# Optimization experiments

Hardware: AMD Instinct MI355X
Metric: run time of the kernel (lower is better)

The kernel has to match this reference:

```python
import jax, jax.numpy as jnp
import numpy as np

EMA = 0.999
EPS = 1e-8


def setup_inputs() -> dict:
    key = jax.random.key(0)
    k1, k2, k3 = jax.random.split(key, 3)
    B, z_dim, H, W = 16, 64, 32, 32
    M = 4096
    N = B * H * W
    return {
        "z": jax.random.normal(k1, (B, z_dim, H, W), dtype=jnp.float32),
        "e": jax.random.normal(k2, (M, z_dim), dtype=jnp.float32),
        "belong": jax.random.uniform(k3, (N, M), dtype=jnp.float32),
        "log_sigma": jnp.zeros((1,), dtype=jnp.float32),
        "max_distance": jnp.ones((1, M), dtype=jnp.float32),
        "distance_p": 2,
    }


def reference(z, e, belong, log_sigma, max_distance, distance_p):
    B, z_dim, H, W = z.shape
    # [B, z_dim, H, W] -> [N, z_dim], N = B*H*W
    zf = jnp.transpose(z, (0, 2, 3, 1)).reshape(-1, z_dim)
    # pairwise L2 distance via GEMM expansion: ||z||^2 + ||e||^2 - 2 z.e
    d2 = (jnp.sum(zf * zf, axis=1, keepdims=True)
          + jnp.sum(e * e, axis=1)[None, :]
          - 2.0 * (zf @ e.T))                      # [N, M]
    distance = jnp.sqrt(jnp.maximum(d2, 0.0))
    # EMA update of per-code max distance (buffer, no grad in original)
    batch_max = jnp.max(belong * distance, axis=0, keepdims=True)  # [1, M]
    new_max = EMA * max_distance + (1.0 - EMA) * batch_max
    new_max = jax.lax.stop_gradient(jnp.clip(new_max, EPS, None))
    p = float(distance_p)
    distance = jnp.where(distance < new_max,
                         distance ** (2.0 / p),
                         distance ** (2.0 * p))
    alpha = -1.0 / (2.0 * jnp.exp(log_sigma) ** 2)  # shape (1,)
    lse = jax.scipy.special.logsumexp(alpha * distance, axis=0)  # [M]
    loss = -jnp.mean(lse) + z_dim * log_sigma  # shape (1,), as in torch
    return loss
```

## Files before the change

kernel.cpp:

```cpp
#include <hip/hip_runtime.h>
#include <hip/hip_bf16.h>

#define ZD   64
#define MM   4096
#define NN   16384
#define HWSZ 1024
#define BB   16

typedef __bf16 bf16x8 __attribute__((ext_vector_type(8)));
typedef float  f32x4  __attribute__((ext_vector_type(4)));

#define EMA_C 0.999f
#define EPS_C 1e-8f

__global__ __launch_bounds__(256) void k_prep_e(const float* __restrict__ e,
                                                __hip_bfloat16* __restrict__ ebf,
                                                float* __restrict__ en2,
                                                unsigned* __restrict__ bmax,
                                                unsigned* __restrict__ dmin,
                                                float* __restrict__ sume) {
    int tid = threadIdx.x;
    int gid = blockIdx.x * 256 + tid;
    if (gid < MM) {
        bmax[gid] = 0u;
        dmin[gid] = 0x7f800000u;
        sume[gid] = 0.f;
    }
    int wave = tid >> 6, lane = tid & 63;
    int row = blockIdx.x * 4 + wave;
    if (row < MM) {
        float v = e[row * ZD + lane];
        __hip_bfloat16 b = __float2bfloat16(v);
        ebf[row * ZD + lane] = b;
        float q = __bfloat162float(b);
        float s = q * q;
        for (int off = 32; off; off >>= 1) s += __shfl_xor(s, off);
        if (lane == 0) en2[row] = s;
    }
}

__global__ __launch_bounds__(256) void k_prep_z(const float* __restrict__ z,
                                                __hip_bfloat16* __restrict__ zf,
                                                float* __restrict__ zn2) {
    __shared__ float tile[64][65];
    __shared__ float part[4][64];
    int b   = blockIdx.x;
    int hw0 = blockIdx.y * 64;
    int tid = threadIdx.x;
    int tx = tid & 63, ty = tid >> 6;
    const float* zp = z + (size_t)b * (ZD * HWSZ);
#pragma unroll
    for (int kk = 0; kk < 16; kk++) {
        int k = kk * 4 + ty;
        tile[k][tx] = zp[(size_t)k * HWSZ + hw0 + tx];
    }
    __syncthreads();
#pragma unroll
    for (int i = 0; i < 16; i++) {
        int li = tid + i * 256;
        int ln = li >> 6, lk = li & 63;
        int n = b * HWSZ + hw0 + ln;
        zf[(size_t)n * ZD + lk] = __float2bfloat16(tile[lk][ln]);
    }
    float s = 0.f;
#pragma unroll
    for (int kk = 0; kk < 16; kk++) {
        float q = __bfloat162float(__float2bfloat16(tile[ty + kk * 4][tx]));
        s += q * q;
    }
    part[ty][tx] = s;
    __syncthreads();
    if (tid < 64) {
        float t = part[0][tid] + part[1][tid] + part[2][tid] + part[3][tid];
        zn2[b * HWSZ + hw0 + tid] = t;
    }
}

__global__ __launch_bounds__(256) void k_pass1(const __hip_bfloat16* __restrict__ zf,
                                               const __hip_bfloat16* __restrict__ ebf,
                                               const float* __restrict__ zn2,
                                               const float* __restrict__ en2,
                                               const float* __restrict__ belong,
                                               unsigned* __restrict__ bmax,
                                               unsigned* __restrict__ dmin) {
    int tid = threadIdx.x;
    int wave = tid >> 6, lane = tid & 63;
    int l16 = lane & 15, lq = lane >> 4;
    int wn = wave >> 1, wm = wave & 1;
    int n0 = blockIdx.x * 64 + wn * 32;
    int m0 = blockIdx.y * 128 + wm * 64;

    const bf16x8* zfv = reinterpret_cast<const bf16x8*>(zf);
    const bf16x8* ebv = reinterpret_cast<const bf16x8*>(ebf);

    bf16x8 Af[2][2], Bf[4][2];
#pragma unroll
    for (int i = 0; i < 2; i++)
#pragma unroll
        for (int h = 0; h < 2; h++)
            Af[i][h] = zfv[(size_t)(n0 + i * 16 + l16) * 8 + h * 4 + lq];
#pragma unroll
    for (int j = 0; j < 4; j++)
#pragma unroll
        for (int h = 0; h < 2; h++)
            Bf[j][h] = ebv[(size_t)(m0 + j * 16 + l16) * 8 + h * 4 + lq];

    f32x4 acc[2][4];
#pragma unroll
    for (int i = 0; i < 2; i++)
#pragma unroll
        for (int j = 0; j < 4; j++) {
            acc[i][j] = (f32x4){0.f, 0.f, 0.f, 0.f};
            acc[i][j] = __builtin_amdgcn_mfma_f32_16x16x32_bf16(Af[i][0], Bf[j][0], acc[i][j], 0, 0, 0);
            acc[i][j] = __builtin_amdgcn_mfma_f32_16x16x32_bf16(Af[i][1], Bf[j][1], acc[i][j], 0, 0, 0);
        }

    float zn2v[2][4];
#pragma unroll
    for (int i = 0; i < 2; i++)
#pragma unroll
        for (int r = 0; r < 4; r++)
            zn2v[i][r] = zn2[n0 + i * 16 + lq * 4 + r];

    __shared__ unsigned smax[128], smin[128];
    if (tid < 128) { smax[tid] = 0u; smin[tid] = 0x7f800000u; }
    __syncthreads();

#pragma unroll
    for (int j = 0; j < 4; j++) {
        float en2v = en2[m0 + j * 16 + l16];
        float vmax = 0.f, vmin = 3.4e38f;
#pragma unroll
        for (int i = 0; i < 2; i++)
#pragma unroll
            for (int r = 0; r < 4; r++) {
                float d2 = zn2v[i][r] + en2v - 2.f * acc[i][j][r];
                float d = sqrtf(fmaxf(d2, 0.f));
                int n = n0 + i * 16 + lq * 4 + r;
                float bel = belong[(size_t)n * MM + (m0 + j * 16 + l16)];
                vmax = fmaxf(vmax, bel * d);
                vmin = fminf(vmin, d);
            }
        vmax = fmaxf(vmax, __shfl_xor(vmax, 16));
        vmax = fmaxf(vmax, __shfl_xor(vmax, 32));
        vmin = fminf(vmin, __shfl_xor(vmin, 16));
        vmin = fminf(vmin, __shfl_xor(vmin, 32));
        if (lane < 16) {
            int ml = wm * 64 + j * 16 + lane;
            atomicMax(&smax[ml], __float_as_uint(vmax));
            atomicMin(&smin[ml], __float_as_uint(vmin));
        }
    }
    __syncthreads();
    if (tid < 128) {
        atomicMax(&bmax[blockIdx.y * 128 + tid], smax[tid]);
        atomicMin(&dmin[blockIdx.y * 128 + tid], smin[tid]);
    }
}

__global__ __launch_bounds__(256) void k_mid(const unsigned* __restrict__ bmax,
                                             const unsigned* __restrict__ dmin,
                                             const float* __restrict__ max_distance,
                                             const float* __restrict__ log_sigma,
                                             const int* __restrict__ pp,
                                             float* __restrict__ nmax,
                                             float* __restrict__ refs) {
    int m = blockIdx.x * 256 + threadIdx.x;
    if (m >= MM) return;
    float bm = __uint_as_float(bmax[m]);
    float dm = __uint_as_float(dmin[m]);
    float nm = fmaxf(EMA_C * max_distance[m] + (1.f - EMA_C) * bm, EPS_C);
    int p = pp[0];
    float tlow;
    if (p == 2) {
        float d4  = (dm * dm) * (dm * dm);
        float nm4 = (nm * nm) * (nm * nm);
        tlow = (dm < nm) ? fminf(dm, nm4) : d4;
    } else {
        float e1 = 2.f / (float)p, e2 = 2.f * (float)p;
        tlow = (dm < nm) ? fminf(powf(dm, e1), powf(nm, e2)) : powf(dm, e2);
    }
    float alpha = -0.5f * expf(-2.f * log_sigma[0]);
    nmax[m] = nm;
    refs[m] = alpha * tlow;
}

__global__ __launch_bounds__(256) void k_pass2(const __hip_bfloat16* __restrict__ zf,
                                               const __hip_bfloat16* __restrict__ ebf,
                                               const float* __restrict__ zn2,
                                               const float* __restrict__ en2,
                                               const float* __restrict__ nmax,
                                               const float* __restrict__ refs,
                                               const float* __restrict__ log_sigma,
                                               const int* __restrict__ pp,
                                               float* __restrict__ sume) {
    int tid = threadIdx.x;
    int wave = tid >> 6, lane = tid & 63;
    int l16 = lane & 15, lq = lane >> 4;
    int wn = wave >> 1, wm = wave & 1;
    int n0 = blockIdx.x * 64 + wn * 32;
    int m0 = blockIdx.y * 128 + wm * 64;

    const bf16x8* zfv = reinterpret_cast<const bf16x8*>(zf);
    const bf16x8* ebv = reinterpret_cast<const bf16x8*>(ebf);

    bf16x8 Af[2][2], Bf[4][2];
#pragma unroll
    for (int i = 0; i < 2; i++)
#pragma unroll
        for (int h = 0; h < 2; h++)
            Af[i][h] = zfv[(size_t)(n0 + i * 16 + l16) * 8 + h * 4 + lq];
#pragma unroll
    for (int j = 0; j < 4; j++)
#pragma unroll
        for (int h = 0; h < 2; h++)
            Bf[j][h] = ebv[(size_t)(m0 + j * 16 + l16) * 8 + h * 4 + lq];

    f32x4 acc[2][4];
#pragma unroll
    for (int i = 0; i < 2; i++)
#pragma unroll
        for (int j = 0; j < 4; j++) {
            acc[i][j] = (f32x4){0.f, 0.f, 0.f, 0.f};
            acc[i][j] = __builtin_amdgcn_mfma_f32_16x16x32_bf16(Af[i][0], Bf[j][0], acc[i][j], 0, 0, 0);
            acc[i][j] = __builtin_amdgcn_mfma_f32_16x16x32_bf16(Af[i][1], Bf[j][1], acc[i][j], 0, 0, 0);
        }

    float zn2v[2][4];
#pragma unroll
    for (int i = 0; i < 2; i++)
#pragma unroll
        for (int r = 0; r < 4; r++)
            zn2v[i][r] = zn2[n0 + i * 16 + lq * 4 + r];

    float alpha = -0.5f * expf(-2.f * log_sigma[0]);
    int p = pp[0];
    bool p2 = (p == 2);
    float e1 = 2.f / (float)p, e2 = 2.f * (float)p;

    __shared__ float ssum[128];
    if (tid < 128) ssum[tid] = 0.f;
    __syncthreads();

#pragma unroll
    for (int j = 0; j < 4; j++) {
        float en2v = en2[m0 + j * 16 + l16];
        float nmv = nmax[m0 + j * 16 + l16];
        float rfv = refs[m0 + j * 16 + l16];
        float csum = 0.f;
#pragma unroll
        for (int i = 0; i < 2; i++)
#pragma unroll
            for (int r = 0; r < 4; r++) {
                float d2c = fmaxf(zn2v[i][r] + en2v - 2.f * acc[i][j][r], 0.f);
                float d = sqrtf(d2c);
                float t;
                if (p2) t = (d < nmv) ? d : d2c * d2c;
                else    t = powf(d, (d < nmv) ? e1 : e2);
                csum += expf(alpha * t - rfv);
            }
        csum += __shfl_xor(csum, 16);
        csum += __shfl_xor(csum, 32);
        if (lane < 16) atomicAdd(&ssum[wm * 64 + j * 16 + lane], csum);
    }
    __syncthreads();
    if (tid < 128) atomicAdd(&sume[blockIdx.y * 128 + tid], ssum[tid]);
}

__global__ __launch_bounds__(256) void k_final(const float* __restrict__ refs,
                                               const float* __restrict__ sume,
                                               const float* __restrict__ log_sigma,
                                               float* __restrict__ out) {
    __shared__ float red[4];
    int tid = threadIdx.x;
    float a = 0.f;
    for (int m = tid; m < MM; m += 256)
        a += refs[m] + logf(fmaxf(sume[m], 1e-30f));
    for (int off = 32; off; off >>= 1) a += __shfl_xor(a, off);
    int wave = tid >> 6, lane = tid & 63;
    if (lane == 0) red[wave] = a;
    __syncthreads();
    if (tid == 0) {
        float t = red[0] + red[1] + red[2] + red[3];
        out[0] = -t / (float)MM + (float)ZD * log_sigma[0];
    }
}

extern "C" void kernel_launch(void* const* d_in, const int* in_sizes, int n_in,
                              void* d_out, int out_size, void* d_ws, size_t ws_size,
                              hipStream_t stream) {
    const float* z            = (const float*)d_in[0];
    const float* e            = (const float*)d_in[1];
    const float* belong       = (const float*)d_in[2];
    const float* log_sigma    = (const float*)d_in[3];
    const float* max_distance = (const float*)d_in[4];
    const int*   pp           = (const int*)d_in[5];
    float* out = (float*)d_out;

    char* ws = (char*)d_ws;
    __hip_bfloat16* zf  = (__hip_bfloat16*)(ws + 0);
    __hip_bfloat16* ebf = (__hip_bfloat16*)(ws + 2097152);
    float*    zn2  = (float*)(ws + 2621440);
    float*    en2  = (float*)(ws + 2686976);
    unsigned* bmax = (unsigned*)(ws + 2703360);
    unsigned* dmin = (unsigned*)(ws + 2719744);
    float*    nmax = (float*)(ws + 2736128);
    float*    refs = (float*)(ws + 2752512);
    float*    sume = (float*)(ws + 2768896);

    k_prep_e<<<1024, 256, 0, stream>>>(e, ebf, en2, bmax, dmin, sume);
    k_prep_z<<<dim3(BB, HWSZ / 64), 256, 0, stream>>>(z, zf, zn2);
    k_pass1<<<dim3(NN / 64, MM / 128), 256, 0, stream>>>(zf, ebf, zn2, en2, belong, bmax, dmin);
    k_mid<<<MM / 256, 256, 0, stream>>>(bmax, dmin, max_distance, log_sigma, pp, nmax, refs);
    k_pass2<<<dim3(NN / 64, MM / 128), 256, 0, stream>>>(zf, ebf, zn2, en2, nmax, refs, log_sigma, pp, sume);
    k_final<<<1, 256, 0, stream>>>(refs, sume, log_sigma, out);
}
```

Before: 503.4 us.

## Transpose pass1 tiling for vectorized belong loads and fuse prep/mid kernels

Pass1 swaps the MFMA operand roles so each lane reads four consecutive belong values as one nontemporal 16-byte load, with the max/min reductions reworked to match the new layout. The two prep kernels are merged into one launch. The mid kernel is folded into pass2, which recomputes the per-code EMA max and reference in shared memory. Pass2 compares squared distances to skip sqrt on one branch and uses fast exp. The aim is to cut launch overhead and make the dominant 256MB belong stream more efficient, at the cost of redundant per-block mid computation and fast-math exp precision.

```diff
diff --git a/kernel.cpp b/kernel.cpp
--- a/kernel.cpp
+++ b/kernel.cpp
@@ -13,66 +13,68 @@
 #define EMA_C 0.999f
 #define EPS_C 1e-8f
 
-__global__ __launch_bounds__(256) void k_prep_e(const float* __restrict__ e,
-                                                __hip_bfloat16* __restrict__ ebf,
-                                                float* __restrict__ en2,
-                                                unsigned* __restrict__ bmax,
-                                                unsigned* __restrict__ dmin,
-                                                float* __restrict__ sume) {
-    int tid = threadIdx.x;
-    int gid = blockIdx.x * 256 + tid;
-    if (gid < MM) {
-        bmax[gid] = 0u;
-        dmin[gid] = 0x7f800000u;
-        sume[gid] = 0.f;
-    }
-    int wave = tid >> 6, lane = tid & 63;
-    int row = blockIdx.x * 4 + wave;
-    if (row < MM) {
-        float v = e[row * ZD + lane];
-        __hip_bfloat16 b = __float2bfloat16(v);
-        ebf[row * ZD + lane] = b;
-        float q = __bfloat162float(b);
-        float s = q * q;
-        for (int off = 32; off; off >>= 1) s += __shfl_xor(s, off);
-        if (lane == 0) en2[row] = s;
-    }
-}
-
-__global__ __launch_bounds__(256) void k_prep_z(const float* __restrict__ z,
-                                                __hip_bfloat16* __restrict__ zf,
-                                                float* __restrict__ zn2) {
+__global__ __launch_bounds__(256) void k_prep(const float* __restrict__ z,
+                                              const float* __restrict__ e,
+                                              __hip_bfloat16* __restrict__ zf,
+                                              __hip_bfloat16* __restrict__ ebf,
+                                              float* __restrict__ zn2,
+                                              float* __restrict__ en2,
+                                              unsigned* __restrict__ bmax,
+                                              unsigned* __restrict__ dmin,
+                                              float* __restrict__ sume) {
     __shared__ float tile[64][65];
     __shared__ float part[4][64];
-    int b   = blockIdx.x;
-    int hw0 = blockIdx.y * 64;
+    int blk = blockIdx.x;
     int tid = threadIdx.x;
-    int tx = tid & 63, ty = tid >> 6;
-    const float* zp = z + (size_t)b * (ZD * HWSZ);
-#pragma unroll
-    for (int kk = 0; kk < 16; kk++) {
-        int k = kk * 4 + ty;
-        tile[k][tx] = zp[(size_t)k * HWSZ + hw0 + tx];
-    }
-    __syncthreads();
-#pragma unroll
-    for (int i = 0; i < 16; i++) {
-        int li = tid + i * 256;
-        int ln = li >> 6, lk = li & 63;
-        int n = b * HWSZ + hw0 + ln;
-        zf[(size_t)n * ZD + lk] = __float2bfloat16(tile[lk][ln]);
-    }
-    float s = 0.f;
-#pragma unroll
-    for (int kk = 0; kk < 16; kk++) {
-        float q = __bfloat162float(__float2bfloat16(tile[ty + kk * 4][tx]));
-        s += q * q;
-    }
-    part[ty][tx] = s;
-    __syncthreads();
-    if (tid < 64) {
-        float t = part[0][tid] + part[1][tid] + part[2][tid] + part[3][tid];
-        zn2[b * HWSZ + hw0 + tid] = t;
+    if (blk < 256) {
+        int b   = blk >> 4;
+        int hw0 = (blk & 15) * 64;
+        int tx = tid & 63, ty = tid >> 6;
+        const float* zp = z + (size_t)b * (ZD * HWSZ);
+#pragma unroll
+        for (int kk = 0; kk < 16; kk++) {
+            int k = kk * 4 + ty;
+            tile[k][tx] = zp[(size_t)k * HWSZ + hw0 + tx];
+        }
+        __syncthreads();
+#pragma unroll
+        for (int i = 0; i < 16; i++) {
+            int li = tid + i * 256;
+            int ln = li >> 6, lk = li & 63;
+            int n = b * HWSZ + hw0 + ln;
+            zf[(size_t)n * ZD + lk] = __float2bfloat16(tile[lk][ln]);
+        }
+        float s = 0.f;
+#pragma unroll
+        for (int kk = 0; kk < 16; kk++) {
+            float q = __bfloat162float(__float2bfloat16(tile[ty * 1 + kk * 4][tx]));
+            s += q * q;
+        }
+        part[ty][tx] = s;
+        __syncthreads();
+        if (tid < 64) {
+            float t = part[0][tid] + part[1][tid] + part[2][tid] + part[3][tid];
+            zn2[b * HWSZ + hw0 + tid] = t;
+        }
+    } else {
+        int eb  = blk - 256;
+        int gid = eb * 256 + tid;
+        if (gid < MM) {
+            bmax[gid] = 0u;
+            dmin[gid] = 0x7f800000u;
+            sume[gid] = 0.f;
+        }
+        int wave = tid >> 6, lane = tid & 63;
+        int row = eb * 4 + wave;
+        if (row < MM) {
+            float v = e[row * ZD + lane];
+            __hip_bfloat16 b16 = __float2bfloat16(v);
+            ebf[row * ZD + lane] = b16;
+            float q = __bfloat162float(b16);
+            float s = q * q;
+            for (int off = 32; off; off >>= 1) s += __shfl_xor(s, off);
+            if (lane == 0) en2[row] = s;
+        }
     }
 }
 
@@ -86,114 +88,114 @@
     int tid = threadIdx.x;
     int wave = tid >> 6, lane = tid & 63;
     int l16 = lane & 15, lq = lane >> 4;
-    int wn = wave >> 1, wm = wave & 1;
-    int n0 = blockIdx.x * 64 + wn * 32;
-    int m0 = blockIdx.y * 128 + wm * 64;
-
+    int wm = wave & 1, wn = wave >> 1;
+    int m0 = blockIdx.x * 64 + wm * 32;
+    int n0 = blockIdx.y * 128 + wn * 64;
+
+    const bf16x8* ebv = reinterpret_cast<const bf16x8*>(ebf);
     const bf16x8* zfv = reinterpret_cast<const bf16x8*>(zf);
-    const bf16x8* ebv = reinterpret_cast<const bf16x8*>(ebf);
 
     bf16x8 Af[2][2], Bf[4][2];
 #pragma unroll
-    for (int i = 0; i < 2; i++)
+    for (int im = 0; im < 2; im++)
 #pragma unroll
         for (int h = 0; h < 2; h++)
-            Af[i][h] = zfv[(size_t)(n0 + i * 16 + l16) * 8 + h * 4 + lq];
-#pragma unroll
-    for (int j = 0; j < 4; j++)
+            Af[im][h] = ebv[(size_t)(m0 + im * 16 + l16) * 8 + h * 4 + lq];
+#pragma unroll
+    for (int jn = 0; jn < 4; jn++)
 #pragma unroll
         for (int h = 0; h < 2; h++)
-            Bf[j][h] = ebv[(size_t)(m0 + j * 16 + l16) * 8 + h * 4 + lq];
+            Bf[jn][h] = zfv[(size_t)(n0 + jn * 16 + l16) * 8 + h * 4 + lq];
+
+    f32x4 bl[2][4];
+#pragma unroll
+    for (int im = 0; im < 2; im++)
+#pragma unroll
+        for (int jn = 0; jn < 4; jn++) {
+            const f32x4* bp = reinterpret_cast<const f32x4*>(
+                belong + (size_t)(n0 + jn * 16 + l16) * MM + (m0 + im * 16 + lq * 4));
+            bl[im][jn] = __builtin_nontemporal_load(bp);
+        }
 
     f32x4 acc[2][4];
 #pragma unroll
-    for (int i = 0; i < 2; i++)
-#pragma unroll
-        for (int j = 0; j < 4; j++) {
-            acc[i][j] = (f32x4){0.f, 0.f, 0.f, 0.f};
-            acc[i][j] = __builtin_amdgcn_mfma_f32_16x16x32_bf16(Af[i][0], Bf[j][0], acc[i][j], 0, 0, 0);
-            acc[i][j] = __builtin_amdgcn_mfma_f32_16x16x32_bf16(Af[i][1], Bf[j][1], acc[i][j], 0, 0, 0);
-        }
-
-    float zn2v[2][4];
-#pragma unroll
-    for (int i = 0; i < 2; i++)
-#pragma unroll
-        for (int r = 0; r < 4; r++)
-            zn2v[i][r] = zn2[n0 + i * 16 + lq * 4 + r];
-
-    __shared__ unsigned smax[128], smin[128];
-    if (tid < 128) { smax[tid] = 0u; smin[tid] = 0x7f800000u; }
-    __syncthreads();
-
-#pragma unroll
-    for (int j = 0; j < 4; j++) {
-        float en2v = en2[m0 + j * 16 + l16];
-        float vmax = 0.f, vmin = 3.4e38f;
-#pragma unroll
-        for (int i = 0; i < 2; i++)
+    for (int im = 0; im < 2; im++)
+#pragma unroll
+        for (int jn = 0; jn < 4; jn++) {
+            acc[im][jn] = (f32x4){0.f, 0.f, 0.f, 0.f};
+            acc[im][jn] = __builtin_amdgcn_mfma_f32_16x16x32_bf16(Af[im][0], Bf[jn][0], acc[im][jn], 0, 0, 0);
+            acc[im][jn] = __builtin_amdgcn_mfma_f32_16x16x32_bf16(Af[im][1], Bf[jn][1], acc[im][jn], 0, 0, 0);
+        }
+
+    f32x4 en2v[2];
+#pragma unroll
+    for (int im = 0; im < 2; im++)
+        en2v[im] = *reinterpret_cast<const f32x4*>(en2 + m0 + im * 16 + lq * 4);
+    float zn2v[4];
+#pragma unroll
+    for (int jn = 0; jn < 4; jn++)
+        zn2v[jn] = zn2[n0 + jn * 16 + l16];
+
+    float vmax[2][4], vmin[2][4];
+#pragma unroll
+    for (int im = 0; im < 2; im++)
+#pragma unroll
+        for (int r = 0; r < 4; r++) { vmax[im][r] = 0.f; vmin[im][r] = 3.4e38f; }
+
+#pragma unroll
+    for (int im = 0; im < 2; im++)
+#pragma unroll
+        for (int jn = 0; jn < 4; jn++)
 #pragma unroll
             for (int r = 0; r < 4; r++) {
-                float d2 = zn2v[i][r] + en2v - 2.f * acc[i][j][r];
+                float d2 = en2v[im][r] + zn2v[jn] - 2.f * acc[im][jn][r];
                 float d = sqrtf(fmaxf(d2, 0.f));
-                int n = n0 + i * 16 + lq * 4 + r;
-                float bel = belong[(size_t)n * MM + (m0 + j * 16 + l16)];
-                vmax = fmaxf(vmax, bel * d);
-                vmin = fminf(vmin, d);
+                vmax[im][r] = fmaxf(vmax[im][r], bl[im][jn][r] * d);
+                vmin[im][r] = fminf(vmin[im][r], d);
             }
-        vmax = fmaxf(vmax, __shfl_xor(vmax, 16));
-        vmax = fmaxf(vmax, __shfl_xor(vmax, 32));
-        vmin = fminf(vmin, __shfl_xor(vmin, 16));
-        vmin = fminf(vmin, __shfl_xor(vmin, 32));
-        if (lane < 16) {
-            int ml = wm * 64 + j * 16 + lane;
-            atomicMax(&smax[ml], __float_as_uint(vmax));
-            atomicMin(&smin[ml], __float_as_uint(vmin));
-        }
-    }
-    __syncthreads();
-    if (tid < 128) {
-        atomicMax(&bmax[blockIdx.y * 128 + tid], smax[tid]);
-        atomicMin(&dmin[blockIdx.y * 128 + tid], smin[tid]);
-    }
-}
-
-__global__ __launch_bounds__(256) void k_mid(const unsigned* __restrict__ bmax,
-                                             const unsigned* __restrict__ dmin,
-                                             const float* __restrict__ max_distance,
-                                             const float* __restrict__ log_sigma,
-                                             const int* __restrict__ pp,
-                                             float* __restrict__ nmax,
-                                             float* __restrict__ refs) {
-    int m = blockIdx.x * 256 + threadIdx.x;
-    if (m >= MM) return;
-    float bm = __uint_as_float(bmax[m]);
-    float dm = __uint_as_float(dmin[m]);
-    float nm = fmaxf(EMA_C * max_distance[m] + (1.f - EMA_C) * bm, EPS_C);
-    int p = pp[0];
-    float tlow;
-    if (p == 2) {
-        float d4  = (dm * dm) * (dm * dm);
-        float nm4 = (nm * nm) * (nm * nm);
-        tlow = (dm < nm) ? fminf(dm, nm4) : d4;
-    } else {
-        float e1 = 2.f / (float)p, e2 = 2.f * (float)p;
-        tlow = (dm < nm) ? fminf(powf(dm, e1), powf(nm, e2)) : powf(dm, e2);
-    }
-    float alpha = -0.5f * expf(-2.f * log_sigma[0]);
-    nmax[m] = nm;
-    refs[m] = alpha * tlow;
+
+#pragma unroll
+    for (int off = 1; off < 16; off <<= 1)
+#pragma unroll
+        for (int im = 0; im < 2; im++)
+#pragma unroll
+            for (int r = 0; r < 4; r++) {
+                vmax[im][r] = fmaxf(vmax[im][r], __shfl_xor(vmax[im][r], off));
+                vmin[im][r] = fminf(vmin[im][r], __shfl_xor(vmin[im][r], off));
+            }
+
+    __shared__ unsigned smax[64], smin[64];
+    if (tid < 64) { smax[tid] = 0u; smin[tid] = 0x7f800000u; }
+    __syncthreads();
+    if (l16 == 0) {
+#pragma unroll
+        for (int im = 0; im < 2; im++)
+#pragma unroll
+            for (int r = 0; r < 4; r++) {
+                int ml = wm * 32 + im * 16 + lq * 4 + r;
+                atomicMax(&smax[ml], __float_as_uint(vmax[im][r]));
+                atomicMin(&smin[ml], __float_as_uint(vmin[im][r]));
+            }
+    }
+    __syncthreads();
+    if (tid < 64) {
+        atomicMax(&bmax[blockIdx.x * 64 + tid], smax[tid]);
+        atomicMin(&dmin[blockIdx.x * 64 + tid], smin[tid]);
+    }
 }
 
 __global__ __launch_bounds__(256) void k_pass2(const __hip_bfloat16* __restrict__ zf,
                                                const __hip_bfloat16* __restrict__ ebf,
                                                const float* __restrict__ zn2,
                                                const float* __restrict__ en2,
-                                               const float* __restrict__ nmax,
-                                               const float* __restrict__ refs,
+                                               const unsigned* __restrict__ bmax,
+                                               const unsigned* __restrict__ dmin,
+                                               const float* __restrict__ max_distance,
                                                const float* __restrict__ log_sigma,
                                                const int* __restrict__ pp,
+                                               float* __restrict__ refs,
                                                float* __restrict__ sume) {
+    __shared__ float snm2[128], sref[128], ssum[128];
     int tid = threadIdx.x;
     int wave = tid >> 6, lane = tid & 63;
     int l16 = lane & 15, lq = lane >> 4;
@@ -201,6 +203,31 @@
     int n0 = blockIdx.x * 64 + wn * 32;
     int m0 = blockIdx.y * 128 + wm * 64;
 
+    int p = pp[0];
+    float alpha = -0.5f * __expf(-2.f * log_sigma[0]);
+
+    if (tid < 128) {
+        int m = blockIdx.y * 128 + tid;
+        float bm = __uint_as_float(bmax[m]);
+        float dm = __uint_as_float(dmin[m]);
+        float nm = fmaxf(EMA_C * max_distance[m] + (1.f - EMA_C) * bm, EPS_C);
+        float tlow;
+        if (p == 2) {
+            float d4  = (dm * dm) * (dm * dm);
+            float nm4 = (nm * nm) * (nm * nm);
+            tlow = (dm < nm) ? fminf(dm, nm4) : d4;
+        } else {
+            float e1 = 2.f / (float)p, e2 = 2.f * (float)p;
+            tlow = (dm < nm) ? fminf(powf(dm, e1), powf(nm, e2)) : powf(dm, e2);
+        }
+        float rf = alpha * tlow;
+        snm2[tid] = nm * nm;
+        sref[tid] = rf;
+        ssum[tid] = 0.f;
+        if (blockIdx.x == 0) refs[m] = rf;
+    }
+    __syncthreads();
+
     const bf16x8* zfv = reinterpret_cast<const bf16x8*>(zf);
     const bf16x8* ebv = reinterpret_cast<const bf16x8*>(ebf);
 
@@ -226,38 +253,29 @@
             acc[i][j] = __builtin_amdgcn_mfma_f32_16x16x32_bf16(Af[i][1], Bf[j][1], acc[i][j], 0, 0, 0);
         }
 
-    float zn2v[2][4];
+    f32x4 zn2v[2];
 #pragma unroll
     for (int i = 0; i < 2; i++)
-#pragma unroll
-        for (int r = 0; r < 4; r++)
-            zn2v[i][r] = zn2[n0 + i * 16 + lq * 4 + r];
-
-    float alpha = -0.5f * expf(-2.f * log_sigma[0]);
-    int p = pp[0];
+        zn2v[i] = *reinterpret_cast<const f32x4*>(zn2 + n0 + i * 16 + lq * 4);
+
     bool p2 = (p == 2);
-    float e1 = 2.f / (float)p, e2 = 2.f * (float)p;
-
-    __shared__ float ssum[128];
-    if (tid < 128) ssum[tid] = 0.f;
-    __syncthreads();
+    float pe = (float)p, pi = 1.f / (float)p;
 
 #pragma unroll
     for (int j = 0; j < 4; j++) {
         float en2v = en2[m0 + j * 16 + l16];
-        float nmv = nmax[m0 + j * 16 + l16];
-        float rfv = refs[m0 + j * 16 + l16];
+        float nm2v = snm2[wm * 64 + j * 16 + l16];
+        float rfv  = sref[wm * 64 + j * 16 + l16];
         float csum = 0.f;
 #pragma unroll
         for (int i = 0; i < 2; i++)
 #pragma unroll
             for (int r = 0; r < 4; r++) {
                 float d2c = fmaxf(zn2v[i][r] + en2v - 2.f * acc[i][j][r], 0.f);
-                float d = sqrtf(d2c);
                 float t;
-                if (p2) t = (d < nmv) ? d : d2c * d2c;
-                else    t = powf(d, (d < nmv) ? e1 : e2);
-                csum += expf(alpha * t - rfv);
+                if (p2) t = (d2c < nm2v) ? sqrtf(d2c) : d2c * d2c;
+                else    t = powf(d2c, (d2c < nm2v) ? pi : pe);
+                csum += __expf(fmaf(alpha, t, -rfv));
             }
         csum += __shfl_xor(csum, 16);
         csum += __shfl_xor(csum, 32);
@@ -304,14 +322,12 @@
     float*    en2  = (float*)(ws + 2686976);
     unsigned* bmax = (unsigned*)(ws + 2703360);
     unsigned* dmin = (unsigned*)(ws + 2719744);
-    float*    nmax = (float*)(ws + 2736128);
-    float*    refs = (float*)(ws + 2752512);
-    float*    sume = (float*)(ws + 2768896);
-
-    k_prep_e<<<1024, 256, 0, stream>>>(e, ebf, en2, bmax, dmin, sume);
-    k_prep_z<<<dim3(BB, HWSZ / 64), 256, 0, stream>>>(z, zf, zn2);
-    k_pass1<<<dim3(NN / 64, MM / 128), 256, 0, stream>>>(zf, ebf, zn2, en2, belong, bmax, dmin);
-    k_mid<<<MM / 256, 256, 0, stream>>>(bmax, dmin, max_distance, log_sigma, pp, nmax, refs);
-    k_pass2<<<dim3(NN / 64, MM / 128), 256, 0, stream>>>(zf, ebf, zn2, en2, nmax, refs, log_sigma, pp, sume);
+    float*    refs = (float*)(ws + 2736128);
+    float*    sume = (float*)(ws + 2752512);
+
+    k_prep<<<1280, 256, 0, stream>>>(z, e, zf, ebf, zn2, en2, bmax, dmin, sume);
+    k_pass1<<<dim3(MM / 64, NN / 128), 256, 0, stream>>>(zf, ebf, zn2, en2, belong, bmax, dmin);
+    k_pass2<<<dim3(NN / 64, MM / 128), 256, 0, stream>>>(zf, ebf, zn2, en2, bmax, dmin,
+                                                         max_distance, log_sigma, pp, refs, sume);
     k_final<<<1, 256, 0, stream>>>(refs, sume, log_sigma, out);
 }
```

Measured after the change: 484.4 us. 3.8% less time.
